# Optimization experiments

Measured on AMD Instinct MI355X. Metric: run time of the kernel, lower is better.

Reference implementation:

```python
import jax, jax.numpy as jnp
import numpy as np

NC = 80        # number of classes
CONF = 0.25    # confidence threshold
RATIO = 0.1    # top-k fraction


def setup_inputs() -> dict:
    key = jax.random.key(0)
    N = 2097152
    data = jax.random.normal(key, (1, N, 4 + NC), dtype=jnp.float32)
    return {"data": data}


def reference(data):
    pred = data[0]                      # [N, 4+nc]
    cls_logits = pred[:, -NC:]          # [N, nc]
    boxes = pred[:, :4]                 # [N, 4]
    scores = jnp.max(cls_logits, axis=1)  # class_id is None -> max over classes
    n = scores.shape[0]
    k = max(1, min(n, int(np.ceil(n * float(RATIO)))))  # static k
    vals, idx = jax.lax.top_k(scores, k)   # [k], [k]
    mask = vals >= CONF                     # [k] bool
    # torch returns 0.0 when mask is empty; masked sums naturally give 0 then.
    loss = jnp.sum(jnp.where(mask, vals, 0.0))
    # output_type == 'all' -> add gathered box sums for masked top-k indices
    loss = loss + jnp.sum(jnp.where(mask[:, None], boxes[idx], 0.0))
    return loss
```

## Files before the change

kernel.cpp:

```cpp
#include <hip/hip_runtime.h>
#include <stdint.h>
#include <math.h>

#define ROWLEN 84
#define F4PR 21
#define RPB 256
#define F4PT (RPB * F4PR)
#define CANDCAP (1u << 21)

__device__ __forceinline__ uint32_t map_f(float f) {
    uint32_t u = __float_as_uint(f);
    return (u & 0x80000000u) ? ~u : (u | 0x80000000u);
}
__device__ __forceinline__ float unmap_f(uint32_t u) {
    uint32_t b = (u & 0x80000000u) ? (u & 0x7FFFFFFFu) : ~u;
    return __uint_as_float(b);
}

__device__ void find_parallel(const uint32_t* hist, int nbins, uint32_t target,
                              uint32_t* s, uint32_t* sc2, uint32_t* outBin, uint32_t* outAbove) {
    int tid = threadIdx.x;
    int chunks = nbins / 256;
    int base = tid * chunks;
    uint32_t part = 0;
    for (int i = 0; i < chunks; ++i) part += hist[base + i];
    s[tid] = part;
    __syncthreads();
    for (int off = 1; off < 256; off <<= 1) {
        uint32_t v = (tid + off < 256) ? s[tid + off] : 0u;
        __syncthreads();
        s[tid] += v;
        __syncthreads();
    }
    uint32_t above_next = (tid < 255) ? s[tid + 1] : 0u;
    bool mine = (s[tid] >= target) && (above_next < target);
    if (mine) { sc2[0] = (uint32_t)tid; sc2[1] = above_next; }
    __syncthreads();
    uint32_t c = sc2[0], above = sc2[1];
    if (tid == 0) {
        uint32_t acc = above;
        int b = (int)c * chunks + chunks - 1;
        for (;; --b) {
            uint32_t hb = hist[b];
            if (acc + hb >= target) break;
            acc += hb;
        }
        sc2[0] = (uint32_t)b;
        sc2[1] = acc;
    }
    __syncthreads();
    *outBin = sc2[0];
    *outAbove = sc2[1];
}

__global__ __launch_bounds__(256) void k_score_hist(const float* __restrict__ pred,
                                                    uint32_t* __restrict__ scores,
                                                    uint32_t* __restrict__ gH1,
                                                    uint32_t* __restrict__ candCnt,
                                                    float* __restrict__ out, int n) {
    __shared__ float pm[F4PT];
    __shared__ uint32_t h[1024];
    int tid = threadIdx.x;
    if (blockIdx.x == 0 && tid == 0) { *out = 0.f; *candCnt = 0u; }
    for (int i = tid; i < 1024; i += 256) h[i] = 0;
    uint32_t tid21 = (uint32_t)tid % 21u;
    const float4* pf4 = (const float4*)pred;
    size_t total_f4 = (size_t)n * F4PR;
    int ntiles = (n + RPB - 1) / RPB;
    for (int tile = blockIdx.x; tile < ntiles; tile += gridDim.x) {
        __syncthreads();
        size_t gbase = (size_t)tile * F4PT;
        int row0 = tile * RPB;
        if (row0 + RPB <= n) {
#pragma unroll
            for (int it = 0; it < F4PR; ++it) {
                const uint32_t BP = (21u - (4u * (uint32_t)it) % 21u) % 21u;
                float4 v = pf4[gbase + it * 256 + tid];
                float m = fmaxf(fmaxf(v.x, v.y), fmaxf(v.z, v.w));
                pm[it * 256 + tid] = (tid21 == BP) ? -INFINITY : m;
            }
        } else {
#pragma unroll
            for (int it = 0; it < F4PR; ++it) {
                const uint32_t BP = (21u - (4u * (uint32_t)it) % 21u) % 21u;
                int l = it * 256 + tid;
                size_t g = gbase + l;
                float m = -INFINITY;
                if (g < total_f4 && tid21 != BP) {
                    float4 v = pf4[g];
                    m = fmaxf(fmaxf(v.x, v.y), fmaxf(v.z, v.w));
                }
                pm[l] = m;
            }
        }
        __syncthreads();
        int row = row0 + tid;
        if (row < n) {
            const float* q = pm + tid * F4PR;
            float m = q[1];
#pragma unroll
            for (int j = 2; j <= 20; ++j) m = fmaxf(m, q[j]);
            uint32_t u = map_f(m);
            scores[row] = u;
            atomicAdd(&h[u >> 22], 1u);
        }
    }
    __syncthreads();
    for (int i = tid; i < 1024; i += 256)
        if (h[i]) atomicAdd(&gH1[i], h[i]);
}

__global__ void k_hist2f(const uint32_t* __restrict__ scores, const uint32_t* __restrict__ gH1,
                         uint32_t* __restrict__ gH2, uint32_t* __restrict__ sres,
                         int n, uint32_t K) {
    __shared__ uint32_t h[2048];
    __shared__ uint32_t s[256];
    __shared__ uint32_t sc2[2];
    for (int i = threadIdx.x; i < 2048; i += 256) h[i] = 0;
    uint32_t bin1, chi1;
    find_parallel(gH1, 1024, K, s, sc2, &bin1, &chi1);
    if (blockIdx.x == 0 && threadIdx.x == 0) { sres[0] = bin1; sres[1] = chi1; }
    int gid = blockIdx.x * 256 + threadIdx.x;
    int stride = gridDim.x * 256;
    const uint4* s4 = (const uint4*)scores;
    int n4 = n >> 2;
    for (int i = gid; i < n4; i += stride) {
        uint4 uu = s4[i];
        if ((uu.x >> 22) == bin1) atomicAdd(&h[(uu.x >> 11) & 0x7FFu], 1u);
        if ((uu.y >> 22) == bin1) atomicAdd(&h[(uu.y >> 11) & 0x7FFu], 1u);
        if ((uu.z >> 22) == bin1) atomicAdd(&h[(uu.z >> 11) & 0x7FFu], 1u);
        if ((uu.w >> 22) == bin1) atomicAdd(&h[(uu.w >> 11) & 0x7FFu], 1u);
    }
    for (int r = n4 * 4 + gid; r < n; r += stride) {
        uint32_t u = scores[r];
        if ((u >> 22) == bin1) atomicAdd(&h[(u >> 11) & 0x7FFu], 1u);
    }
    __syncthreads();
    for (int i = threadIdx.x; i < 2048; i += 256)
        if (h[i]) atomicAdd(&gH2[i], h[i]);
}

__global__ void k_select2(const float* __restrict__ pred, const uint32_t* __restrict__ scores,
                          const uint32_t* __restrict__ gH2, uint32_t* __restrict__ sres,
                          uint32_t* __restrict__ candCnt, unsigned long long* __restrict__ candBuf,
                          float* __restrict__ out, int n, uint32_t K) {
    __shared__ uint32_t s[256];
    __shared__ uint32_t sc2[2];
    __shared__ float wsum[4];
    int tid = threadIdx.x;
    uint32_t bin1 = sres[0], chi1 = sres[1];
    uint32_t bin2, chi2;
    find_parallel(gH2, 2048, K - chi1, s, sc2, &bin2, &chi2);
    uint32_t t21 = (bin1 << 11) | bin2;
    uint32_t chiTot = chi1 + chi2;
    uint32_t mprime = K - chiTot;
    if (blockIdx.x == 0 && tid == 0) { sres[2] = t21; sres[4] = mprime; }
    const uint32_t u_conf = 0xBE800000u;
    const uint32_t CONF21 = u_conf >> 11;
    bool tcut = (t21 >= CONF21);
    float lsum = 0.f;
    int gid = blockIdx.x * 256 + tid;
    int stride = gridDim.x * 256;
    const uint4* s4 = (const uint4*)scores;
    int n4 = n >> 2;
    for (int i = gid; i < n4; i += stride) {
        uint4 uu = s4[i];
#pragma unroll
        for (int j = 0; j < 4; ++j) {
            uint32_t u = (j == 0) ? uu.x : (j == 1) ? uu.y : (j == 2) ? uu.z : uu.w;
            int r = i * 4 + j;
            bool sel = tcut ? ((u >> 11) > t21) : (u >= u_conf);
            if (sel) {
                float4 b = *(const float4*)(pred + (size_t)r * ROWLEN);
                lsum += unmap_f(u) + b.x + b.y + b.z + b.w;
            }
            if (tcut && (u >> 11) == t21) {
                uint32_t pos = atomicAdd(candCnt, 1u);
                if (pos < CANDCAP)
                    candBuf[pos] = ((unsigned long long)u << 32) | (uint32_t)r;
            }
        }
    }
    for (int r = n4 * 4 + gid; r < n; r += stride) {
        uint32_t u = scores[r];
        bool sel = tcut ? ((u >> 11) > t21) : (u >= u_conf);
        if (sel) {
            float4 b = *(const float4*)(pred + (size_t)r * ROWLEN);
            lsum += unmap_f(u) + b.x + b.y + b.z + b.w;
        }
        if (tcut && (u >> 11) == t21) {
            uint32_t pos = atomicAdd(candCnt, 1u);
            if (pos < CANDCAP)
                candBuf[pos] = ((unsigned long long)u << 32) | (uint32_t)r;
        }
    }
    for (int off = 32; off; off >>= 1) lsum += __shfl_down(lsum, off);
    int wid = tid >> 6, lane = tid & 63;
    if (lane == 0) wsum[wid] = lsum;
    __syncthreads();
    if (tid == 0) atomicAdd(out, wsum[0] + wsum[1] + wsum[2] + wsum[3]);
}

__global__ void k_final(const float* __restrict__ pred, const uint32_t* __restrict__ sres,
                        const uint32_t* __restrict__ candCnt,
                        const unsigned long long* __restrict__ candBuf,
                        float* __restrict__ out) {
    __shared__ uint32_t h[2048];
    __shared__ uint32_t s[256];
    __shared__ uint32_t sc2[2];
    __shared__ float wsum[4];
    __shared__ uint32_t tb[1024];
    __shared__ uint32_t tc;
    uint32_t t21 = sres[2];
    const uint32_t u_conf = 0xBE800000u;
    const uint32_t CONF21 = u_conf >> 11;
    if (t21 < CONF21) return;
    uint32_t mprime = sres[4];
    uint32_t cc = *candCnt;
    if (cc > CANDCAP) cc = CANDCAP;
    int tid = threadIdx.x;
    for (int i = tid; i < 2048; i += 256) h[i] = 0;
    if (tid == 0) tc = 0;
    __syncthreads();
    for (uint32_t i = tid; i < cc; i += 256)
        atomicAdd(&h[(uint32_t)(candBuf[i] >> 32) & 0x7FFu], 1u);
    __syncthreads();
    uint32_t bin3, chi3;
    find_parallel(h, 2048, mprime, s, sc2, &bin3, &chi3);
    uint32_t t_u = (t21 << 11) | bin3;
    uint32_t mt = mprime - chi3;
    float fsum = 0.f;
    for (uint32_t i = tid; i < cc; i += 256) {
        unsigned long long v = candBuf[i];
        uint32_t key = (uint32_t)(v >> 32);
        uint32_t r = (uint32_t)v;
        uint32_t low = key & 0x7FFu;
        if (low > bin3) {
            float4 b = *(const float4*)(pred + (size_t)r * ROWLEN);
            fsum += unmap_f(key) + b.x + b.y + b.z + b.w;
        } else if (low == bin3) {
            uint32_t p = atomicAdd(&tc, 1u);
            if (p < 1024) tb[p] = r;
        }
    }
    __syncthreads();
    uint32_t tcnt = tc;
    if (tcnt > 1024) tcnt = 1024;
    if (mt >= tcnt) {
        for (uint32_t i = tid; i < tcnt; i += 256) {
            float4 b = *(const float4*)(pred + (size_t)tb[i] * ROWLEN);
            fsum += b.x + b.y + b.z + b.w;
        }
    } else {
        for (uint32_t i = tid; i < tcnt; i += 256) {
            uint32_t ri = tb[i];
            uint32_t rank = 0;
            for (uint32_t j = 0; j < tcnt; ++j) rank += (tb[j] < ri) ? 1u : 0u;
            if (rank < mt) {
                float4 b = *(const float4*)(pred + (size_t)ri * ROWLEN);
                fsum += b.x + b.y + b.z + b.w;
            }
        }
    }
    for (int off = 32; off; off >>= 1) fsum += __shfl_down(fsum, off);
    int wid = tid >> 6, lane = tid & 63;
    if (lane == 0) wsum[wid] = fsum;
    __syncthreads();
    if (tid == 0)
        atomicAdd(out, wsum[0] + wsum[1] + wsum[2] + wsum[3] + (float)mt * unmap_f(t_u));
}

extern "C" void kernel_launch(void* const* d_in, const int* in_sizes, int n_in,
                              void* d_out, int out_size, void* d_ws, size_t ws_size,
                              hipStream_t stream) {
    const float* pred = (const float*)d_in[0];
    int n = in_sizes[0] / ROWLEN;
    double kd = ceil((double)n * 0.1);
    long kk = (long)kd;
    if (kk < 1) kk = 1;
    if (kk > n) kk = n;
    uint32_t K = (uint32_t)kk;

    uint32_t* ws32 = (uint32_t*)d_ws;
    uint32_t* scores = ws32;
    uint32_t* gH1 = ws32 + n;
    uint32_t* gH2 = gH1 + 1024;
    uint32_t* candCnt = gH2 + 2048;
    uint32_t* sres = candCnt + 16;
    unsigned long long* candBuf = (unsigned long long*)(sres + 16);
    float* out = (float*)d_out;

    hipMemsetAsync(gH1, 0, (1024 + 2048) * sizeof(uint32_t), stream);

    k_score_hist<<<2048, 256, 0, stream>>>(pred, scores, gH1, candCnt, out, n);
    k_hist2f<<<1024, 256, 0, stream>>>(scores, gH1, gH2, sres, n, K);
    k_select2<<<2048, 256, 0, stream>>>(pred, scores, gH2, sres, candCnt, candBuf, out, n, K);
    k_final<<<1, 256, 0, stream>>>(pred, sres, candCnt, candBuf, out);
}
```

Measured before the change: 195.4 us.

## Precompute per-row box sums in score pass and use wave-shuffle suffix scan

The first pass now computes each row's box-coordinate sum while it streams the input and writes it to a compact workspace array. The select and final kernels then read this contiguous float array instead of gathering strided 16-byte box chunks from the large prediction tensor. This turns roughly 210k scattered gathers into a coalesced 8 MB stream, at the cost of an extra 8 MB write in the first pass. The threshold-finding prefix scan also switches from a shared-memory loop with many barriers to wavefront shuffles plus a small cross-wave combine.

```diff
diff --git a/kernel.cpp b/kernel.cpp
--- a/kernel.cpp
+++ b/kernel.cpp
@@ -18,27 +18,31 @@
 }
 
 __device__ void find_parallel(const uint32_t* hist, int nbins, uint32_t target,
-                              uint32_t* s, uint32_t* sc2, uint32_t* outBin, uint32_t* outAbove) {
-    int tid = threadIdx.x;
+                              uint32_t* swt, uint32_t* sc2,
+                              uint32_t* outBin, uint32_t* outAbove) {
+    int tid = threadIdx.x;
+    int lane = tid & 63, wv = tid >> 6;
     int chunks = nbins / 256;
     int base = tid * chunks;
     uint32_t part = 0;
     for (int i = 0; i < chunks; ++i) part += hist[base + i];
-    s[tid] = part;
-    __syncthreads();
-    for (int off = 1; off < 256; off <<= 1) {
-        uint32_t v = (tid + off < 256) ? s[tid + off] : 0u;
-        __syncthreads();
-        s[tid] += v;
-        __syncthreads();
-    }
-    uint32_t above_next = (tid < 255) ? s[tid + 1] : 0u;
-    bool mine = (s[tid] >= target) && (above_next < target);
-    if (mine) { sc2[0] = (uint32_t)tid; sc2[1] = above_next; }
-    __syncthreads();
-    uint32_t c = sc2[0], above = sc2[1];
+    uint32_t sfx = part;
+#pragma unroll
+    for (int off = 1; off < 64; off <<= 1) {
+        uint32_t v = __shfl_down(sfx, off);
+        if (lane + off < 64) sfx += v;
+    }
+    if (lane == 0) swt[wv] = sfx;
+    __syncthreads();
+    uint32_t add = 0;
+    for (int w = wv + 1; w < 4; ++w) add += swt[w];
+    uint32_t suffix = sfx + add;
+    uint32_t above = suffix - part;
+    if (suffix >= target && above < target) { sc2[0] = (uint32_t)tid; sc2[1] = above; }
+    __syncthreads();
+    uint32_t c = sc2[0];
     if (tid == 0) {
-        uint32_t acc = above;
+        uint32_t acc = sc2[1];
         int b = (int)c * chunks + chunks - 1;
         for (;; --b) {
             uint32_t hb = hist[b];
@@ -55,6 +59,7 @@
 
 __global__ __launch_bounds__(256) void k_score_hist(const float* __restrict__ pred,
                                                     uint32_t* __restrict__ scores,
+                                                    float* __restrict__ bsum,
                                                     uint32_t* __restrict__ gH1,
                                                     uint32_t* __restrict__ candCnt,
                                                     float* __restrict__ out, int n) {
@@ -77,7 +82,8 @@
                 const uint32_t BP = (21u - (4u * (uint32_t)it) % 21u) % 21u;
                 float4 v = pf4[gbase + it * 256 + tid];
                 float m = fmaxf(fmaxf(v.x, v.y), fmaxf(v.z, v.w));
-                pm[it * 256 + tid] = (tid21 == BP) ? -INFINITY : m;
+                float sB = v.x + v.y + v.z + v.w;
+                pm[it * 256 + tid] = (tid21 == BP) ? sB : m;
             }
         } else {
 #pragma unroll
@@ -85,10 +91,11 @@
                 const uint32_t BP = (21u - (4u * (uint32_t)it) % 21u) % 21u;
                 int l = it * 256 + tid;
                 size_t g = gbase + l;
-                float m = -INFINITY;
-                if (g < total_f4 && tid21 != BP) {
+                float m = 0.f;
+                if (g < total_f4) {
                     float4 v = pf4[g];
-                    m = fmaxf(fmaxf(v.x, v.y), fmaxf(v.z, v.w));
+                    m = (tid21 == BP) ? (v.x + v.y + v.z + v.w)
+                                      : fmaxf(fmaxf(v.x, v.y), fmaxf(v.z, v.w));
                 }
                 pm[l] = m;
             }
@@ -97,11 +104,13 @@
         int row = row0 + tid;
         if (row < n) {
             const float* q = pm + tid * F4PR;
+            float bs = q[0];
             float m = q[1];
 #pragma unroll
             for (int j = 2; j <= 20; ++j) m = fmaxf(m, q[j]);
             uint32_t u = map_f(m);
             scores[row] = u;
+            bsum[row] = bs;
             atomicAdd(&h[u >> 22], 1u);
         }
     }
@@ -114,11 +123,12 @@
                          uint32_t* __restrict__ gH2, uint32_t* __restrict__ sres,
                          int n, uint32_t K) {
     __shared__ uint32_t h[2048];
-    __shared__ uint32_t s[256];
+    __shared__ uint32_t swt[4];
     __shared__ uint32_t sc2[2];
     for (int i = threadIdx.x; i < 2048; i += 256) h[i] = 0;
+    __syncthreads();
     uint32_t bin1, chi1;
-    find_parallel(gH1, 1024, K, s, sc2, &bin1, &chi1);
+    find_parallel(gH1, 1024, K, swt, sc2, &bin1, &chi1);
     if (blockIdx.x == 0 && threadIdx.x == 0) { sres[0] = bin1; sres[1] = chi1; }
     int gid = blockIdx.x * 256 + threadIdx.x;
     int stride = gridDim.x * 256;
@@ -140,17 +150,17 @@
         if (h[i]) atomicAdd(&gH2[i], h[i]);
 }
 
-__global__ void k_select2(const float* __restrict__ pred, const uint32_t* __restrict__ scores,
+__global__ void k_select2(const uint32_t* __restrict__ scores, const float* __restrict__ bsum,
                           const uint32_t* __restrict__ gH2, uint32_t* __restrict__ sres,
                           uint32_t* __restrict__ candCnt, unsigned long long* __restrict__ candBuf,
                           float* __restrict__ out, int n, uint32_t K) {
-    __shared__ uint32_t s[256];
+    __shared__ uint32_t swt[4];
     __shared__ uint32_t sc2[2];
     __shared__ float wsum[4];
     int tid = threadIdx.x;
     uint32_t bin1 = sres[0], chi1 = sres[1];
     uint32_t bin2, chi2;
-    find_parallel(gH2, 2048, K - chi1, s, sc2, &bin2, &chi2);
+    find_parallel(gH2, 2048, K - chi1, swt, sc2, &bin2, &chi2);
     uint32_t t21 = (bin1 << 11) | bin2;
     uint32_t chiTot = chi1 + chi2;
     uint32_t mprime = K - chiTot;
@@ -162,32 +172,28 @@
     int gid = blockIdx.x * 256 + tid;
     int stride = gridDim.x * 256;
     const uint4* s4 = (const uint4*)scores;
+    const float4* b4 = (const float4*)bsum;
     int n4 = n >> 2;
     for (int i = gid; i < n4; i += stride) {
         uint4 uu = s4[i];
+        float4 bb = b4[i];
 #pragma unroll
         for (int j = 0; j < 4; ++j) {
             uint32_t u = (j == 0) ? uu.x : (j == 1) ? uu.y : (j == 2) ? uu.z : uu.w;
-            int r = i * 4 + j;
+            float bv = (j == 0) ? bb.x : (j == 1) ? bb.y : (j == 2) ? bb.z : bb.w;
             bool sel = tcut ? ((u >> 11) > t21) : (u >= u_conf);
-            if (sel) {
-                float4 b = *(const float4*)(pred + (size_t)r * ROWLEN);
-                lsum += unmap_f(u) + b.x + b.y + b.z + b.w;
-            }
+            if (sel) lsum += unmap_f(u) + bv;
             if (tcut && (u >> 11) == t21) {
                 uint32_t pos = atomicAdd(candCnt, 1u);
                 if (pos < CANDCAP)
-                    candBuf[pos] = ((unsigned long long)u << 32) | (uint32_t)r;
+                    candBuf[pos] = ((unsigned long long)u << 32) | (uint32_t)(i * 4 + j);
             }
         }
     }
     for (int r = n4 * 4 + gid; r < n; r += stride) {
         uint32_t u = scores[r];
         bool sel = tcut ? ((u >> 11) > t21) : (u >= u_conf);
-        if (sel) {
-            float4 b = *(const float4*)(pred + (size_t)r * ROWLEN);
-            lsum += unmap_f(u) + b.x + b.y + b.z + b.w;
-        }
+        if (sel) lsum += unmap_f(u) + bsum[r];
         if (tcut && (u >> 11) == t21) {
             uint32_t pos = atomicAdd(candCnt, 1u);
             if (pos < CANDCAP)
@@ -201,12 +207,12 @@
     if (tid == 0) atomicAdd(out, wsum[0] + wsum[1] + wsum[2] + wsum[3]);
 }
 
-__global__ void k_final(const float* __restrict__ pred, const uint32_t* __restrict__ sres,
+__global__ void k_final(const float* __restrict__ bsum, const uint32_t* __restrict__ sres,
                         const uint32_t* __restrict__ candCnt,
                         const unsigned long long* __restrict__ candBuf,
                         float* __restrict__ out) {
     __shared__ uint32_t h[2048];
-    __shared__ uint32_t s[256];
+    __shared__ uint32_t swt[4];
     __shared__ uint32_t sc2[2];
     __shared__ float wsum[4];
     __shared__ uint32_t tb[1024];
@@ -226,7 +232,7 @@
         atomicAdd(&h[(uint32_t)(candBuf[i] >> 32) & 0x7FFu], 1u);
     __syncthreads();
     uint32_t bin3, chi3;
-    find_parallel(h, 2048, mprime, s, sc2, &bin3, &chi3);
+    find_parallel(h, 2048, mprime, swt, sc2, &bin3, &chi3);
     uint32_t t_u = (t21 << 11) | bin3;
     uint32_t mt = mprime - chi3;
     float fsum = 0.f;
@@ -236,8 +242,7 @@
         uint32_t r = (uint32_t)v;
         uint32_t low = key & 0x7FFu;
         if (low > bin3) {
-            float4 b = *(const float4*)(pred + (size_t)r * ROWLEN);
-            fsum += unmap_f(key) + b.x + b.y + b.z + b.w;
+            fsum += unmap_f(key) + bsum[r];
         } else if (low == bin3) {
             uint32_t p = atomicAdd(&tc, 1u);
             if (p < 1024) tb[p] = r;
@@ -247,19 +252,13 @@
     uint32_t tcnt = tc;
     if (tcnt > 1024) tcnt = 1024;
     if (mt >= tcnt) {
-        for (uint32_t i = tid; i < tcnt; i += 256) {
-            float4 b = *(const float4*)(pred + (size_t)tb[i] * ROWLEN);
-            fsum += b.x + b.y + b.z + b.w;
-        }
+        for (uint32_t i = tid; i < tcnt; i += 256) fsum += bsum[tb[i]];
     } else {
         for (uint32_t i = tid; i < tcnt; i += 256) {
             uint32_t ri = tb[i];
             uint32_t rank = 0;
             for (uint32_t j = 0; j < tcnt; ++j) rank += (tb[j] < ri) ? 1u : 0u;
-            if (rank < mt) {
-                float4 b = *(const float4*)(pred + (size_t)ri * ROWLEN);
-                fsum += b.x + b.y + b.z + b.w;
-            }
+            if (rank < mt) fsum += bsum[ri];
         }
     }
     for (int off = 32; off; off >>= 1) fsum += __shfl_down(fsum, off);
@@ -283,7 +282,8 @@
 
     uint32_t* ws32 = (uint32_t*)d_ws;
     uint32_t* scores = ws32;
-    uint32_t* gH1 = ws32 + n;
+    float* bsum = (float*)(ws32 + n);
+    uint32_t* gH1 = ws32 + 2 * (size_t)n;
     uint32_t* gH2 = gH1 + 1024;
     uint32_t* candCnt = gH2 + 2048;
     uint32_t* sres = candCnt + 16;
@@ -292,8 +292,8 @@
 
     hipMemsetAsync(gH1, 0, (1024 + 2048) * sizeof(uint32_t), stream);
 
-    k_score_hist<<<2048, 256, 0, stream>>>(pred, scores, gH1, candCnt, out, n);
+    k_score_hist<<<2048, 256, 0, stream>>>(pred, scores, bsum, gH1, candCnt, out, n);
     k_hist2f<<<1024, 256, 0, stream>>>(scores, gH1, gH2, sres, n, K);
-    k_select2<<<2048, 256, 0, stream>>>(pred, scores, gH2, sres, candCnt, candBuf, out, n, K);
-    k_final<<<1, 256, 0, stream>>>(pred, sres, candCnt, candBuf, out);
-}
+    k_select2<<<2048, 256, 0, stream>>>(scores, bsum, gH2, sres, candCnt, candBuf, out, n, K);
+    k_final<<<1, 256, 0, stream>>>(bsum, sres, candCnt, candBuf, out);
+}
```

Result: no change. 198.7 us (+1.7%).
